# Optimization experiments

Measured on AMD Instinct MI355X. Metric: run time of the kernel, lower is better.

Reference implementation:

```python
import jax, jax.numpy as jnp
import numpy as np

HV = 128          # hidden_value_dim
HT = 17           # hidden_type_dim
K = HT - 9        # number of per-type composition linears (8)
D = 2 * (HV + HT) # gate-linear input dim (290)
O = 5 * HV        # gate-linear output dim (640)
P = 400_000       # child-state pool size
N = 200_000       # number of parent compositions


def setup_inputs() -> dict:
    key = jax.random.key(0)
    ks = jax.random.split(key, 7)
    h_pool = jax.random.normal(ks[0], (P, HV), dtype=jnp.float32)
    c_pool = jax.random.normal(ks[1], (P, HV), dtype=jnp.float32)
    # soft type distributions per child (gumbel-softmax outputs in the original)
    t_pool = jax.random.uniform(ks[2], (P, HT), dtype=jnp.float32)
    child_idx = jax.random.randint(ks[3], (N, 2), 0, P)
    parent_type = jax.random.randint(ks[4], (N,), 0, K)
    # per-type composition weights (comp_linear_v), orthogonal-ish init -> plain normal scaled
    W = jax.random.normal(ks[5], (K, O, D), dtype=jnp.float32) / np.sqrt(D)
    b = jnp.zeros((K, O), dtype=jnp.float32)
    return {"h_pool": h_pool, "c_pool": c_pool, "t_pool": t_pool,
            "child_idx": child_idx, "parent_type": parent_type,
            "W": W, "b": b}


def _compose(h_pool, c_pool, t_pool, child_idx, parent_type, W, b):
    # gather children states  [N, hv] / [N, ht]
    li, ri = child_idx[:, 0], child_idx[:, 1]
    hl, hr = h_pool[li], h_pool[ri]
    cl, cr = c_pool[li], c_pool[ri]
    tl, tr = t_pool[li], t_pool[ri]
    # per-type linear input: concat(hl, tl, hr, tr)  [N, D]
    x = jnp.concatenate([hl, tl, hr, tr], axis=-1)
    # per-type gates via masked accumulation over the small fixed set of K types
    gates = jnp.zeros((x.shape[0], O), dtype=x.dtype)
    for k in range(K):
        yk = x @ W[k].T + b[k]                       # [N, O]
        gates = jnp.where((parent_type == k)[:, None], yk, gates)
    # binary tree-LSTM cell update: i, f_l, f_r, u, o
    i, fl, fr, u, o = jnp.split(gates, 5, axis=-1)
    c = (jax.nn.sigmoid(i) * jnp.tanh(u)
         + jax.nn.sigmoid(fl) * cl
         + jax.nn.sigmoid(fr) * cr)
    h = jax.nn.sigmoid(o) * jnp.tanh(c)
    return jnp.concatenate([h, c], axis=-1)         # [N, 2*hv]


def reference(h_pool, c_pool, t_pool, child_idx, parent_type, W, b):
    return _compose(h_pool, c_pool, t_pool, child_idx, parent_type, W, b)
```

## Files before the change

### kernel.cpp

```cpp
#include <hip/hip_runtime.h>
#include <hip/hip_bf16.h>

#define HV   128
#define HT   17
#define DIMD 290
#define KP   320
#define OO   640
#define RT   64
#define KN   8

typedef unsigned short u16;
typedef __attribute__((ext_vector_type(8))) short short8v;
typedef __attribute__((ext_vector_type(4))) float f32x4;

__device__ __forceinline__ u16 f2bf(float x) {
    unsigned u = __float_as_uint(x);
    u = (u + 0x7FFFu + ((u >> 16) & 1u)) >> 16;
    return (u16)u;
}
__device__ __forceinline__ float sigf(float x) {
    return __builtin_amdgcn_rcpf(1.0f + __expf(-x));
}
__device__ __forceinline__ float tanhfast(float x) {
    return 1.0f - 2.0f * __builtin_amdgcn_rcpf(1.0f + __expf(2.0f * x));
}


__global__ void hist_k(const int* __restrict__ pt, int* __restrict__ hdr, int N) {
    __shared__ int c[KN];
    if (threadIdx.x < KN) c[threadIdx.x] = 0;
    __syncthreads();
    int n = blockIdx.x * 256 + threadIdx.x;
    if (n < N) atomicAdd(&c[pt[n]], 1);
    __syncthreads();
    if (threadIdx.x < KN && c[threadIdx.x]) atomicAdd(&hdr[threadIdx.x], c[threadIdx.x]);
}

__global__ void prefix_k(int* __restrict__ hdr) {
    if (threadIdx.x == 0 && blockIdx.x == 0) {
        int acc = 0;
        hdr[16] = 0;
        for (int k = 0; k < KN; ++k) {
            acc += (hdr[k] + RT - 1) / RT;
            hdr[17 + k] = acc;
        }
    }
}

__global__ void scatter_k(const int* __restrict__ pt, int* __restrict__ hdr,
                          int* __restrict__ idxbuf, int N) {
    __shared__ int c[KN], base[KN];
    if (threadIdx.x < KN) c[threadIdx.x] = 0;
    __syncthreads();
    int n = blockIdx.x * 256 + threadIdx.x;
    int k = 0, my = 0;
    if (n < N) { k = pt[n]; my = atomicAdd(&c[k], 1); }
    __syncthreads();
    if (threadIdx.x < KN)
        base[threadIdx.x] = c[threadIdx.x] ? atomicAdd(&hdr[8 + threadIdx.x], c[threadIdx.x]) : 0;
    __syncthreads();
    if (n < N) idxbuf[hdr[16 + k] * RT + base[k] + my] = n;
}

__global__ void wconv_k(const float* __restrict__ W, u16* __restrict__ Wt) {
    int k = blockIdx.y;
    int idx = blockIdx.x * 256 + threadIdx.x;
    if (idx >= OO * KP) return;
    int o = idx / KP, d = idx % KP;
    int src;
    if (d < 256)      src = (d < 128) ? d : d + 17;
    else if (d < 273) src = d - 128;
    else if (d < 290) src = d;
    else              src = -1;
    float v = (src >= 0) ? W[((size_t)k * OO + o) * DIMD + src] : 0.0f;
    int kk = d >> 5, e = d & 31;
    Wt[(((size_t)k * 10 + kk) * OO + o) * 32 + e] = f2bf(v);
}

__global__ __launch_bounds__(512, 2)
void fused_k(const float* __restrict__ h_pool, const float* __restrict__ c_pool,
             const float* __restrict__ t_pool, const int* __restrict__ child_idx,
             const float* __restrict__ bias, const u16* __restrict__ Wt,
             const int* __restrict__ hdr, const int* __restrict__ idxbuf,
             float* __restrict__ out) {
    __shared__ u16 sX[RT * KP];
    __shared__ int4 sMeta[2][RT];

    const int ntiles = hdr[24];
    const int t0 = blockIdx.x * 2;
    if (t0 >= ntiles) return;
    const int t1 = t0 + 1;
    const bool has1 = (t1 < ntiles);

    const int tid = threadIdx.x;
    const int r = tid >> 3, q = tid & 7;

    float4 A0[4], B0[4];
    float Tl0, Tl1, Tl2 = 0.f, Tr0, Tr1, Tr2 = 0.f;
    int sn, sl, sr2;

    auto loadmeta = [&](int tile) {
        sn = idxbuf[tile * RT + r];
        sl = 0; sr2 = 0;
        if (sn >= 0) { sl = child_idx[2 * sn]; sr2 = child_idx[2 * sn + 1]; }
    };
    auto issue_stage = [&]() {
        if (sn < 0) return;
        const float4* hl = (const float4*)(h_pool + (size_t)sl * HV);
        const float4* hr = (const float4*)(h_pool + (size_t)sr2 * HV);
        #pragma unroll
        for (int m = 0; m < 4; ++m) A0[m] = hl[q + 8 * m];
        #pragma unroll
        for (int m = 0; m < 4; ++m) B0[m] = hr[q + 8 * m];
        const float* tl = t_pool + (size_t)sl * HT;
        const float* tr = t_pool + (size_t)sr2 * HT;
        Tl0 = tl[q]; Tl1 = tl[q + 8];
        Tr0 = tr[q]; Tr1 = tr[q + 8];
        if (q == 0) { Tl2 = tl[16]; Tr2 = tr[16]; }
    };
    auto write_stage = [&]() {
        char* xr = (char*)sX + r * 640;
        const int swz = (r & 7) << 4;
        if (sn >= 0) {
            #pragma unroll
            for (int m = 0; m < 4; ++m) {
                float4 v = A0[m];
                *(ushort4*)(xr + (((q + 8 * m) * 8) ^ swz)) =
                    make_ushort4(f2bf(v.x), f2bf(v.y), f2bf(v.z), f2bf(v.w));
            }
            #pragma unroll
            for (int m = 0; m < 4; ++m) {
                float4 v = B0[m];
                *(ushort4*)(xr + ((256 + (q + 8 * m) * 8) ^ swz)) =
                    make_ushort4(f2bf(v.x), f2bf(v.y), f2bf(v.z), f2bf(v.w));
            }
            *(u16*)(xr + ((512 + 2 * q) ^ swz))       = f2bf(Tl0);
            *(u16*)(xr + ((512 + 2 * (q + 8)) ^ swz)) = f2bf(Tl1);
            *(u16*)(xr + ((546 + 2 * q) ^ swz))       = f2bf(Tr0);
            *(u16*)(xr + ((546 + 2 * (q + 8)) ^ swz)) = f2bf(Tr1);
            if (q == 0) {
                *(u16*)(xr + (544 ^ swz)) = f2bf(Tl2);
                *(u16*)(xr + (578 ^ swz)) = f2bf(Tr2);
            }
            for (int b = 580 + 2 * q; b < 640; b += 16)
                *(u16*)(xr + (b ^ swz)) = 0;
        } else {
            ushort4 z = make_ushort4(0, 0, 0, 0);
            for (int b = q * 8; b < 640; b += 64)
                *(ushort4*)(xr + (b ^ swz)) = z;
        }
    };

    loadmeta(t0);
    if (q == 0) sMeta[0][r] = make_int4(sn, sl, sr2, 0);
    issue_stage();
    write_stage();
    __syncthreads();

    const int wc = tid >> 6, lane = tid & 63;
    const int lo = lane & 15, hi = lane >> 4;
    const int hcol = wc * 16 + lo;
    const char* sXb = (const char*)sX;
    const int rowbase = lo * 640;
    const int swzl = (lo & 7) << 4;

    if (has1) {
        loadmeta(t1);
        if (q == 0) sMeta[1][r] = make_int4(sn, sl, sr2, 0);
        issue_stage();
    }

    int k0 = 0;
    #pragma unroll
    for (int j = 0; j < 7; ++j) k0 += (t0 >= hdr[17 + j]);

    int nodes[16];
    float cpl[16], cpr[16];
    #pragma unroll
    for (int m = 0; m < 4; ++m)
        #pragma unroll
        for (int jj = 0; jj < 4; ++jj) {
            int4 mt = sMeta[0][m * 16 + hi * 4 + jj];
            nodes[m * 4 + jj] = mt.x;
            cpl[m * 4 + jj] = c_pool[(size_t)mt.y * HV + hcol];
            cpr[m * 4 + jj] = c_pool[(size_t)mt.z * HV + hcol];
        }
    float bb[5];
    #pragma unroll
    for (int g = 0; g < 5; ++g) bb[g] = bias[k0 * OO + g * 128 + hcol];

    int wo[5];
    #pragma unroll
    for (int g = 0; g < 5; ++g)
        wo[g] = (g * 128 + hcol) * 32 + hi * 8;

    {
        f32x4 acc[5][4];
        #pragma unroll
        for (int g = 0; g < 5; ++g)
            #pragma unroll
            for (int m = 0; m < 4; ++m)
                acc[g][m] = (f32x4){0.f, 0.f, 0.f, 0.f};

        const u16* __restrict__ wt = Wt + ((size_t)k0 * 10 * OO) * 32;
        short8v wfa[5], wfb[5];
        #pragma unroll
        for (int g = 0; g < 5; ++g) wfa[g] = *(const short8v*)(wt + wo[g]);

        #pragma unroll
        for (int kk = 0; kk < 10; ++kk) {
            short8v (&wcur)[5] = (kk & 1) ? wfb : wfa;
            short8v (&wnxt)[5] = (kk & 1) ? wfa : wfb;
            if (kk < 9) {
                const u16* wtn = wt + (size_t)(kk + 1) * (OO * 32);
                #pragma unroll
                for (int g = 0; g < 5; ++g)
                    wnxt[g] = *(const short8v*)(wtn + wo[g]);
            }
            int a_off = rowbase + ((kk * 64 + hi * 16) ^ swzl);
            short8v a0 = *(const short8v*)(sXb + a_off);
            short8v a1 = *(const short8v*)(sXb + a_off + 10240);
            short8v a2 = *(const short8v*)(sXb + a_off + 20480);
            short8v a3 = *(const short8v*)(sXb + a_off + 30720);
            #pragma unroll
            for (int g = 0; g < 5; ++g) {
                acc[g][0] = __builtin_amdgcn_mfma_f32_16x16x32_bf16(a0, wcur[g], acc[g][0], 0, 0, 0);
                acc[g][1] = __builtin_amdgcn_mfma_f32_16x16x32_bf16(a1, wcur[g], acc[g][1], 0, 0, 0);
                acc[g][2] = __builtin_amdgcn_mfma_f32_16x16x32_bf16(a2, wcur[g], acc[g][2], 0, 0, 0);
                acc[g][3] = __builtin_amdgcn_mfma_f32_16x16x32_bf16(a3, wcur[g], acc[g][3], 0, 0, 0);
            }
        }

        #pragma unroll
        for (int m = 0; m < 4; ++m) {
            #pragma unroll
            for (int jj = 0; jj < 4; ++jj) {
                int node = nodes[m * 4 + jj];
                if (node < 0) continue;
                float cl = cpl[m * 4 + jj], cr = cpr[m * 4 + jj];
                float gi  = acc[0][m][jj] + bb[0];
                float gfl = acc[1][m][jj] + bb[1];
                float gfr = acc[2][m][jj] + bb[2];
                float gu  = acc[3][m][jj] + bb[3];
                float go  = acc[4][m][jj] + bb[4];
                float cc = sigf(gi) * tanhfast(gu) + sigf(gfl) * cl + sigf(gfr) * cr;
                float hh = sigf(go) * tanhfast(cc);
                float* orow = out + (size_t)node * (2 * HV);
                orow[hcol]      = hh;
                orow[HV + hcol] = cc;
            }
        }
    }

    if (!has1) return;

    __syncthreads();
    write_stage();
    __syncthreads();

    int k1 = 0;
    #pragma unroll
    for (int j = 0; j < 7; ++j) k1 += (t1 >= hdr[17 + j]);

    #pragma unroll
    for (int m = 0; m < 4; ++m)
        #pragma unroll
        for (int jj = 0; jj < 4; ++jj) {
            int4 mt = sMeta[1][m * 16 + hi * 4 + jj];
            nodes[m * 4 + jj] = mt.x;
            cpl[m * 4 + jj] = c_pool[(size_t)mt.y * HV + hcol];
            cpr[m * 4 + jj] = c_pool[(size_t)mt.z * HV + hcol];
        }
    #pragma unroll
    for (int g = 0; g < 5; ++g) bb[g] = bias[k1 * OO + g * 128 + hcol];

    {
        f32x4 acc[5][4];
        #pragma unroll
        for (int g = 0; g < 5; ++g)
            #pragma unroll
            for (int m = 0; m < 4; ++m)
                acc[g][m] = (f32x4){0.f, 0.f, 0.f, 0.f};

        const u16* __restrict__ wt = Wt + ((size_t)k1 * 10 * OO) * 32;
        short8v wfa[5], wfb[5];
        #pragma unroll
        for (int g = 0; g < 5; ++g) wfa[g] = *(const short8v*)(wt + wo[g]);

        #pragma unroll
        for (int kk = 0; kk < 10; ++kk) {
            short8v (&wcur)[5] = (kk & 1) ? wfb : wfa;
            short8v (&wnxt)[5] = (kk & 1) ? wfa : wfb;
            if (kk < 9) {
                const u16* wtn = wt + (size_t)(kk + 1) * (OO * 32);
                #pragma unroll
                for (int g = 0; g < 5; ++g)
                    wnxt[g] = *(const short8v*)(wtn + wo[g]);
            }
            int a_off = rowbase + ((kk * 64 + hi * 16) ^ swzl);
            short8v a0 = *(const short8v*)(sXb + a_off);
            short8v a1 = *(const short8v*)(sXb + a_off + 10240);
            short8v a2 = *(const short8v*)(sXb + a_off + 20480);
            short8v a3 = *(const short8v*)(sXb + a_off + 30720);
            #pragma unroll
            for (int g = 0; g < 5; ++g) {
                acc[g][0] = __builtin_amdgcn_mfma_f32_16x16x32_bf16(a0, wcur[g], acc[g][0], 0, 0, 0);
                acc[g][1] = __builtin_amdgcn_mfma_f32_16x16x32_bf16(a1, wcur[g], acc[g][1], 0, 0, 0);
                acc[g][2] = __builtin_amdgcn_mfma_f32_16x16x32_bf16(a2, wcur[g], acc[g][2], 0, 0, 0);
                acc[g][3] = __builtin_amdgcn_mfma_f32_16x16x32_bf16(a3, wcur[g], acc[g][3], 0, 0, 0);
            }
        }

        #pragma unroll
        for (int m = 0; m < 4; ++m) {
            #pragma unroll
            for (int jj = 0; jj < 4; ++jj) {
                int node = nodes[m * 4 + jj];
                if (node < 0) continue;
                float cl = cpl[m * 4 + jj], cr = cpr[m * 4 + jj];
                float gi  = acc[0][m][jj] + bb[0];
                float gfl = acc[1][m][jj] + bb[1];
                float gfr = acc[2][m][jj] + bb[2];
                float gu  = acc[3][m][jj] + bb[3];
                float go  = acc[4][m][jj] + bb[4];
                float cc = sigf(gi) * tanhfast(gu) + sigf(gfl) * cl + sigf(gfr) * cr;
                float hh = sigf(go) * tanhfast(cc);
                float* orow = out + (size_t)node * (2 * HV);
                orow[hcol]      = hh;
                orow[HV + hcol] = cc;
            }
        }
    }
}

extern "C" void kernel_launch(void* const* d_in, const int* in_sizes, int n_in,
                              void* d_out, int out_size, void* d_ws, size_t ws_size,
                              hipStream_t stream) {
    const float* h_pool      = (const float*)d_in[0];
    const float* c_pool      = (const float*)d_in[1];
    const float* t_pool      = (const float*)d_in[2];
    const int*   child_idx   = (const int*)d_in[3];
    const int*   parent_type = (const int*)d_in[4];
    const float* W           = (const float*)d_in[5];
    const float* bias        = (const float*)d_in[6];
    float* out = (float*)d_out;

    const int N = in_sizes[3] / 2;
    const int maxblk = (N + RT - 1) / RT + KN;
    const int totrows = maxblk * RT;

    char* ws = (char*)d_ws;
    size_t off = 0;
    int* hdr = (int*)ws;                         off += 1024;
    int* idxbuf = (int*)(ws + off);              off += (((size_t)totrows * 4 + 255) / 256) * 256;
    u16* Wt = (u16*)(ws + off);                  off += (size_t)KN * OO * KP * 2;

    hipMemsetAsync(hdr, 0, 1024, stream);
    hipMemsetAsync(idxbuf, 0xFF, (size_t)totrows * 4, stream);

    int nb = (N + 255) / 256;
    hist_k<<<nb, 256, 0, stream>>>(parent_type, hdr, N);
    prefix_k<<<1, 64, 0, stream>>>(hdr);
    scatter_k<<<nb, 256, 0, stream>>>(parent_type, hdr, idxbuf, N);
    wconv_k<<<dim3((OO * KP + 255) / 256, KN), 256, 0, stream>>>(W, Wt);
    fused_k<<<(maxblk + 1) / 2, 512, 0, stream>>>(
        h_pool, c_pool, t_pool, child_idx, bias, Wt, hdr, idxbuf, out);
}
```

Baseline: 321.9 us.

## Make fused kernel persistent with double-buffered LDS tile pipeline

```diff
diff --git a/kernel.cpp b/kernel.cpp
--- a/kernel.cpp
+++ b/kernel.cpp
@@ -8,6 +8,7 @@
 #define OO   640
 #define RT   64
 #define KN   8
+#define GG   256
 
 typedef unsigned short u16;
 typedef __attribute__((ext_vector_type(8))) short short8v;
@@ -78,19 +79,17 @@
 }
 
 __global__ __launch_bounds__(512, 2)
-void fused_k(const float* __restrict__ h_pool, const float* __restrict__ c_pool,
-             const float* __restrict__ t_pool, const int* __restrict__ child_idx,
-             const float* __restrict__ bias, const u16* __restrict__ Wt,
-             const int* __restrict__ hdr, const int* __restrict__ idxbuf,
-             float* __restrict__ out) {
-    __shared__ u16 sX[RT * KP];
+void fusedp_k(const float* __restrict__ h_pool, const float* __restrict__ c_pool,
+              const float* __restrict__ t_pool, const int* __restrict__ child_idx,
+              const float* __restrict__ bias, const u16* __restrict__ Wt,
+              const int* __restrict__ hdr, const int* __restrict__ idxbuf,
+              float* __restrict__ out) {
+    __shared__ u16 sX[2][RT * KP];
     __shared__ int4 sMeta[2][RT];
 
     const int ntiles = hdr[24];
-    const int t0 = blockIdx.x * 2;
-    if (t0 >= ntiles) return;
-    const int t1 = t0 + 1;
-    const bool has1 = (t1 < ntiles);
+    const int bx = blockIdx.x;
+    if (bx >= ntiles) return;
 
     const int tid = threadIdx.x;
     const int r = tid >> 3, q = tid & 7;
@@ -118,8 +117,8 @@
         Tr0 = tr[q]; Tr1 = tr[q + 8];
         if (q == 0) { Tl2 = tl[16]; Tr2 = tr[16]; }
     };
-    auto write_stage = [&]() {
-        char* xr = (char*)sX + r * 640;
+    auto write_stage = [&](int pb) {
+        char* xr = (char*)sX[pb] + r * 640;
         const int swz = (r & 7) << 4;
         if (sn >= 0) {
             #pragma unroll
@@ -151,50 +150,51 @@
         }
     };
 
-    loadmeta(t0);
+    loadmeta(bx);
     if (q == 0) sMeta[0][r] = make_int4(sn, sl, sr2, 0);
     issue_stage();
-    write_stage();
+    write_stage(0);
+    if (bx + GG < ntiles) { loadmeta(bx + GG); issue_stage(); }
     __syncthreads();
 
     const int wc = tid >> 6, lane = tid & 63;
     const int lo = lane & 15, hi = lane >> 4;
     const int hcol = wc * 16 + lo;
-    const char* sXb = (const char*)sX;
     const int rowbase = lo * 640;
     const int swzl = (lo & 7) << 4;
-
-    if (has1) {
-        loadmeta(t1);
-        if (q == 0) sMeta[1][r] = make_int4(sn, sl, sr2, 0);
-        issue_stage();
-    }
-
-    int k0 = 0;
-    #pragma unroll
-    for (int j = 0; j < 7; ++j) k0 += (t0 >= hdr[17 + j]);
-
-    int nodes[16];
-    float cpl[16], cpr[16];
-    #pragma unroll
-    for (int m = 0; m < 4; ++m)
-        #pragma unroll
-        for (int jj = 0; jj < 4; ++jj) {
-            int4 mt = sMeta[0][m * 16 + hi * 4 + jj];
-            nodes[m * 4 + jj] = mt.x;
-            cpl[m * 4 + jj] = c_pool[(size_t)mt.y * HV + hcol];
-            cpr[m * 4 + jj] = c_pool[(size_t)mt.z * HV + hcol];
-        }
-    float bb[5];
-    #pragma unroll
-    for (int g = 0; g < 5; ++g) bb[g] = bias[k0 * OO + g * 128 + hcol];
-
     int wo[5];
     #pragma unroll
     for (int g = 0; g < 5; ++g)
         wo[g] = (g * 128 + hcol) * 32 + hi * 8;
 
-    {
+    int p = 0;
+    for (int t = bx; t < ntiles; t += GG) {
+        const char* sXb = (const char*)sX[p];
+
+        int k = 0;
+        #pragma unroll
+        for (int j = 0; j < 7; ++j) k += (t >= hdr[17 + j]);
+
+        float cpl[16], cpr[16];
+        #pragma unroll
+        for (int m = 0; m < 4; ++m)
+            #pragma unroll
+            for (int jj = 0; jj < 4; ++jj) {
+                int4 mt = sMeta[p][m * 16 + hi * 4 + jj];
+                cpl[m * 4 + jj] = c_pool[(size_t)mt.y * HV + hcol];
+                cpr[m * 4 + jj] = c_pool[(size_t)mt.z * HV + hcol];
+            }
+        float bb[5];
+        #pragma unroll
+        for (int g = 0; g < 5; ++g) bb[g] = bias[k * OO + g * 128 + hcol];
+
+        const bool hasn1 = (t + GG < ntiles);
+        if (hasn1) {
+            if (q == 0) sMeta[p ^ 1][r] = make_int4(sn, sl, sr2, 0);
+            write_stage(p ^ 1);
+        }
+        if (t + 2 * GG < ntiles) { loadmeta(t + 2 * GG); issue_stage(); }
+
         f32x4 acc[5][4];
         #pragma unroll
         for (int g = 0; g < 5; ++g)
@@ -202,7 +202,7 @@
             for (int m = 0; m < 4; ++m)
                 acc[g][m] = (f32x4){0.f, 0.f, 0.f, 0.f};
 
-        const u16* __restrict__ wt = Wt + ((size_t)k0 * 10 * OO) * 32;
+        const u16* __restrict__ wt = Wt + ((size_t)k * 10 * OO) * 32;
         short8v wfa[5], wfb[5];
         #pragma unroll
         for (int g = 0; g < 5; ++g) wfa[g] = *(const short8v*)(wt + wo[g]);
@@ -235,8 +235,8 @@
         for (int m = 0; m < 4; ++m) {
             #pragma unroll
             for (int jj = 0; jj < 4; ++jj) {
-                int node = nodes[m * 4 + jj];
-                if (node < 0) continue;
+                int4 mt = sMeta[p][m * 16 + hi * 4 + jj];
+                if (mt.x < 0) continue;
                 float cl = cpl[m * 4 + jj], cr = cpr[m * 4 + jj];
                 float gi  = acc[0][m][jj] + bb[0];
                 float gfl = acc[1][m][jj] + bb[1];
@@ -245,90 +245,16 @@
                 float go  = acc[4][m][jj] + bb[4];
                 float cc = sigf(gi) * tanhfast(gu) + sigf(gfl) * cl + sigf(gfr) * cr;
                 float hh = sigf(go) * tanhfast(cc);
-                float* orow = out + (size_t)node * (2 * HV);
+                float* orow = out + (size_t)mt.x * (2 * HV);
                 orow[hcol]      = hh;
                 orow[HV + hcol] = cc;
             }
         }
-    }
-
-    if (!has1) return;
-
-    __syncthreads();
-    write_stage();
-    __syncthreads();
-
-    int k1 = 0;
-    #pragma unroll
-    for (int j = 0; j < 7; ++j) k1 += (t1 >= hdr[17 + j]);
-
-    #pragma unroll
-    for (int m = 0; m < 4; ++m)
-        #pragma unroll
-        for (int jj = 0; jj < 4; ++jj) {
-            int4 mt = sMeta[1][m * 16 + hi * 4 + jj];
-            nodes[m * 4 + jj] = mt.x;
-            cpl[m * 4 + jj] = c_pool[(size_t)mt.y * HV + hcol];
-            cpr[m * 4 + jj] = c_pool[(size_t)mt.z * HV + hcol];
-        }
-    #pragma unroll
-    for (int g = 0; g < 5; ++g) bb[g] = bias[k1 * OO + g * 128 + hcol];
-
-    {
-        f32x4 acc[5][4];
-        #pragma unroll
-        for (int g = 0; g < 5; ++g)
-            #pragma unroll
-            for (int m = 0; m < 4; ++m)
-                acc[g][m] = (f32x4){0.f, 0.f, 0.f, 0.f};
-
-        const u16* __restrict__ wt = Wt + ((size_t)k1 * 10 * OO) * 32;
-        short8v wfa[5], wfb[5];
-        #pragma unroll
-        for (int g = 0; g < 5; ++g) wfa[g] = *(const short8v*)(wt + wo[g]);
-
-        #pragma unroll
-        for (int kk = 0; kk < 10; ++kk) {
-            short8v (&wcur)[5] = (kk & 1) ? wfb : wfa;
-            short8v (&wnxt)[5] = (kk & 1) ? wfa : wfb;
-            if (kk < 9) {
-                const u16* wtn = wt + (size_t)(kk + 1) * (OO * 32);
-                #pragma unroll
-                for (int g = 0; g < 5; ++g)
-                    wnxt[g] = *(const short8v*)(wtn + wo[g]);
-            }
-            int a_off = rowbase + ((kk * 64 + hi * 16) ^ swzl);
-            short8v a0 = *(const short8v*)(sXb + a_off);
-            short8v a1 = *(const short8v*)(sXb + a_off + 10240);
-            short8v a2 = *(const short8v*)(sXb + a_off + 20480);
-            short8v a3 = *(const short8v*)(sXb + a_off + 30720);
-            #pragma unroll
-            for (int g = 0; g < 5; ++g) {
-                acc[g][0] = __builtin_amdgcn_mfma_f32_16x16x32_bf16(a0, wcur[g], acc[g][0], 0, 0, 0);
-                acc[g][1] = __builtin_amdgcn_mfma_f32_16x16x32_bf16(a1, wcur[g], acc[g][1], 0, 0, 0);
-                acc[g][2] = __builtin_amdgcn_mfma_f32_16x16x32_bf16(a2, wcur[g], acc[g][2], 0, 0, 0);
-                acc[g][3] = __builtin_amdgcn_mfma_f32_16x16x32_bf16(a3, wcur[g], acc[g][3], 0, 0, 0);
-            }
-        }
-
-        #pragma unroll
-        for (int m = 0; m < 4; ++m) {
-            #pragma unroll
-            for (int jj = 0; jj < 4; ++jj) {
-                int node = nodes[m * 4 + jj];
-                if (node < 0) continue;
-                float cl = cpl[m * 4 + jj], cr = cpr[m * 4 + jj];
-                float gi  = acc[0][m][jj] + bb[0];
-                float gfl = acc[1][m][jj] + bb[1];
-                float gfr = acc[2][m][jj] + bb[2];
-                float gu  = acc[3][m][jj] + bb[3];
-                float go  = acc[4][m][jj] + bb[4];
-                float cc = sigf(gi) * tanhfast(gu) + sigf(gfl) * cl + sigf(gfr) * cr;
-                float hh = sigf(go) * tanhfast(cc);
-                float* orow = out + (size_t)node * (2 * HV);
-                orow[hcol]      = hh;
-                orow[HV + hcol] = cc;
-            }
+
+        if (hasn1) {
+            asm volatile("s_waitcnt lgkmcnt(0)" ::: "memory");
+            __builtin_amdgcn_s_barrier();
+            p ^= 1;
         }
     }
 }
@@ -363,6 +289,6 @@
     prefix_k<<<1, 64, 0, stream>>>(hdr);
     scatter_k<<<nb, 256, 0, stream>>>(parent_type, hdr, idxbuf, N);
     wconv_k<<<dim3((OO * KP + 255) / 256, KN), 256, 0, stream>>>(W, Wt);
-    fused_k<<<(maxblk + 1) / 2, 512, 0, stream>>>(
+    fusedp_k<<<GG, 512, 0, stream>>>(
         h_pool, c_pool, t_pool, child_idx, bias, Wt, hdr, idxbuf, out);
 }
```

Result: no change. 324.3 us (+0.7%).

## Split tile rows across two wave groups with 1024-thread blocks

Applied to the files above, without the earlier changes.

```diff
diff --git a/kernel.cpp b/kernel.cpp
--- a/kernel.cpp
+++ b/kernel.cpp
@@ -77,12 +77,12 @@
     Wt[(((size_t)k * 10 + kk) * OO + o) * 32 + e] = f2bf(v);
 }
 
-__global__ __launch_bounds__(512, 2)
-void fused_k(const float* __restrict__ h_pool, const float* __restrict__ c_pool,
-             const float* __restrict__ t_pool, const int* __restrict__ child_idx,
-             const float* __restrict__ bias, const u16* __restrict__ Wt,
-             const int* __restrict__ hdr, const int* __restrict__ idxbuf,
-             float* __restrict__ out) {
+__global__ __launch_bounds__(1024, 4)
+void fused2_k(const float* __restrict__ h_pool, const float* __restrict__ c_pool,
+              const float* __restrict__ t_pool, const int* __restrict__ child_idx,
+              const float* __restrict__ bias, const u16* __restrict__ Wt,
+              const int* __restrict__ hdr, const int* __restrict__ idxbuf,
+              float* __restrict__ out) {
     __shared__ u16 sX[RT * KP];
     __shared__ int4 sMeta[2][RT];
 
@@ -93,10 +93,10 @@
     const bool has1 = (t1 < ntiles);
 
     const int tid = threadIdx.x;
-    const int r = tid >> 3, q = tid & 7;
-
-    float4 A0[4], B0[4];
-    float Tl0, Tl1, Tl2 = 0.f, Tr0, Tr1, Tr2 = 0.f;
+    const int r = tid >> 4, q = tid & 15;
+
+    float4 A0[2], B0[2];
+    float Tl0, Tl2 = 0.f, Tr0, Tr2 = 0.f;
     int sn, sl, sr2;
 
     auto loadmeta = [&](int tile) {
@@ -109,13 +109,12 @@
         const float4* hl = (const float4*)(h_pool + (size_t)sl * HV);
         const float4* hr = (const float4*)(h_pool + (size_t)sr2 * HV);
         #pragma unroll
-        for (int m = 0; m < 4; ++m) A0[m] = hl[q + 8 * m];
-        #pragma unroll
-        for (int m = 0; m < 4; ++m) B0[m] = hr[q + 8 * m];
+        for (int m = 0; m < 2; ++m) A0[m] = hl[q + 16 * m];
+        #pragma unroll
+        for (int m = 0; m < 2; ++m) B0[m] = hr[q + 16 * m];
         const float* tl = t_pool + (size_t)sl * HT;
         const float* tr = t_pool + (size_t)sr2 * HT;
-        Tl0 = tl[q]; Tl1 = tl[q + 8];
-        Tr0 = tr[q]; Tr1 = tr[q + 8];
+        Tl0 = tl[q]; Tr0 = tr[q];
         if (q == 0) { Tl2 = tl[16]; Tr2 = tr[16]; }
     };
     auto write_stage = [&]() {
@@ -123,30 +122,28 @@
         const int swz = (r & 7) << 4;
         if (sn >= 0) {
             #pragma unroll
-            for (int m = 0; m < 4; ++m) {
+            for (int m = 0; m < 2; ++m) {
                 float4 v = A0[m];
-                *(ushort4*)(xr + (((q + 8 * m) * 8) ^ swz)) =
+                *(ushort4*)(xr + (((q + 16 * m) * 8) ^ swz)) =
                     make_ushort4(f2bf(v.x), f2bf(v.y), f2bf(v.z), f2bf(v.w));
             }
             #pragma unroll
-            for (int m = 0; m < 4; ++m) {
+            for (int m = 0; m < 2; ++m) {
                 float4 v = B0[m];
-                *(ushort4*)(xr + ((256 + (q + 8 * m) * 8) ^ swz)) =
+                *(ushort4*)(xr + ((256 + (q + 16 * m) * 8) ^ swz)) =
                     make_ushort4(f2bf(v.x), f2bf(v.y), f2bf(v.z), f2bf(v.w));
             }
-            *(u16*)(xr + ((512 + 2 * q) ^ swz))       = f2bf(Tl0);
-            *(u16*)(xr + ((512 + 2 * (q + 8)) ^ swz)) = f2bf(Tl1);
-            *(u16*)(xr + ((546 + 2 * q) ^ swz))       = f2bf(Tr0);
-            *(u16*)(xr + ((546 + 2 * (q + 8)) ^ swz)) = f2bf(Tr1);
+            *(u16*)(xr + ((512 + 2 * q) ^ swz)) = f2bf(Tl0);
+            *(u16*)(xr + ((546 + 2 * q) ^ swz)) = f2bf(Tr0);
             if (q == 0) {
                 *(u16*)(xr + (544 ^ swz)) = f2bf(Tl2);
                 *(u16*)(xr + (578 ^ swz)) = f2bf(Tr2);
             }
-            for (int b = 580 + 2 * q; b < 640; b += 16)
+            for (int b = 580 + 2 * q; b < 640; b += 32)
                 *(u16*)(xr + (b ^ swz)) = 0;
         } else {
             ushort4 z = make_ushort4(0, 0, 0, 0);
-            for (int b = q * 8; b < 640; b += 64)
+            for (int b = q * 8; b < 640; b += 128)
                 *(ushort4*)(xr + (b ^ swz)) = z;
         }
     };
@@ -157,11 +154,12 @@
     write_stage();
     __syncthreads();
 
-    const int wc = tid >> 6, lane = tid & 63;
+    const int w = tid >> 6, lane = tid & 63;
+    const int rg = w >> 3, c0 = w & 7;
     const int lo = lane & 15, hi = lane >> 4;
-    const int hcol = wc * 16 + lo;
+    const int hcol = c0 * 16 + lo;
     const char* sXb = (const char*)sX;
-    const int rowbase = lo * 640;
+    const int rowbase0 = (rg * 32 + lo) * 640;
     const int swzl = (lo & 7) << 4;
 
     if (has1) {
@@ -174,16 +172,16 @@
     #pragma unroll
     for (int j = 0; j < 7; ++j) k0 += (t0 >= hdr[17 + j]);
 
-    int nodes[16];
-    float cpl[16], cpr[16];
-    #pragma unroll
-    for (int m = 0; m < 4; ++m)
+    int nodes[8];
+    float cpl[8], cpr[8];
+    #pragma unroll
+    for (int f = 0; f < 2; ++f)
         #pragma unroll
         for (int jj = 0; jj < 4; ++jj) {
-            int4 mt = sMeta[0][m * 16 + hi * 4 + jj];
-            nodes[m * 4 + jj] = mt.x;
-            cpl[m * 4 + jj] = c_pool[(size_t)mt.y * HV + hcol];
-            cpr[m * 4 + jj] = c_pool[(size_t)mt.z * HV + hcol];
+            int4 mt = sMeta[0][rg * 32 + f * 16 + hi * 4 + jj];
+            nodes[f * 4 + jj] = mt.x;
+            cpl[f * 4 + jj] = c_pool[(size_t)mt.y * HV + hcol];
+            cpr[f * 4 + jj] = c_pool[(size_t)mt.z * HV + hcol];
         }
     float bb[5];
     #pragma unroll
@@ -195,12 +193,12 @@
         wo[g] = (g * 128 + hcol) * 32 + hi * 8;
 
     {
-        f32x4 acc[5][4];
+        f32x4 acc[5][2];
         #pragma unroll
         for (int g = 0; g < 5; ++g)
             #pragma unroll
-            for (int m = 0; m < 4; ++m)
-                acc[g][m] = (f32x4){0.f, 0.f, 0.f, 0.f};
+            for (int f = 0; f < 2; ++f)
+                acc[g][f] = (f32x4){0.f, 0.f, 0.f, 0.f};
 
         const u16* __restrict__ wt = Wt + ((size_t)k0 * 10 * OO) * 32;
         short8v wfa[5], wfb[5];
@@ -217,32 +215,28 @@
                 for (int g = 0; g < 5; ++g)
                     wnxt[g] = *(const short8v*)(wtn + wo[g]);
             }
-            int a_off = rowbase + ((kk * 64 + hi * 16) ^ swzl);
+            int a_off = rowbase0 + ((kk * 64 + hi * 16) ^ swzl);
             short8v a0 = *(const short8v*)(sXb + a_off);
             short8v a1 = *(const short8v*)(sXb + a_off + 10240);
-            short8v a2 = *(const short8v*)(sXb + a_off + 20480);
-            short8v a3 = *(const short8v*)(sXb + a_off + 30720);
             #pragma unroll
             for (int g = 0; g < 5; ++g) {
                 acc[g][0] = __builtin_amdgcn_mfma_f32_16x16x32_bf16(a0, wcur[g], acc[g][0], 0, 0, 0);
                 acc[g][1] = __builtin_amdgcn_mfma_f32_16x16x32_bf16(a1, wcur[g], acc[g][1], 0, 0, 0);
-                acc[g][2] = __builtin_amdgcn_mfma_f32_16x16x32_bf16(a2, wcur[g], acc[g][2], 0, 0, 0);
-                acc[g][3] = __builtin_amdgcn_mfma_f32_16x16x32_bf16(a3, wcur[g], acc[g][3], 0, 0, 0);
-            }
-        }
-
-        #pragma unroll
-        for (int m = 0; m < 4; ++m) {
+            }
+        }
+
+        #pragma unroll
+        for (int f = 0; f < 2; ++f) {
             #pragma unroll
             for (int jj = 0; jj < 4; ++jj) {
-                int node = nodes[m * 4 + jj];
+                int node = nodes[f * 4 + jj];
                 if (node < 0) continue;
-                float cl = cpl[m * 4 + jj], cr = cpr[m * 4 + jj];
-                float gi  = acc[0][m][jj] + bb[0];
-                float gfl = acc[1][m][jj] + bb[1];
-                float gfr = acc[2][m][jj] + bb[2];
-                float gu  = acc[3][m][jj] + bb[3];
-                float go  = acc[4][m][jj] + bb[4];
+                float cl = cpl[f * 4 + jj], cr = cpr[f * 4 + jj];
+                float gi  = acc[0][f][jj] + bb[0];
+                float gfl = acc[1][f][jj] + bb[1];
+                float gfr = acc[2][f][jj] + bb[2];
+                float gu  = acc[3][f][jj] + bb[3];
+                float go  = acc[4][f][jj] + bb[4];
                 float cc = sigf(gi) * tanhfast(gu) + sigf(gfl) * cl + sigf(gfr) * cr;
                 float hh = sigf(go) * tanhfast(cc);
                 float* orow = out + (size_t)node * (2 * HV);
@@ -263,24 +257,24 @@
     for (int j = 0; j < 7; ++j) k1 += (t1 >= hdr[17 + j]);
 
     #pragma unroll
-    for (int m = 0; m < 4; ++m)
+    for (int f = 0; f < 2; ++f)
         #pragma unroll
         for (int jj = 0; jj < 4; ++jj) {
-            int4 mt = sMeta[1][m * 16 + hi * 4 + jj];
-            nodes[m * 4 + jj] = mt.x;
-            cpl[m * 4 + jj] = c_pool[(size_t)mt.y * HV + hcol];
-            cpr[m * 4 + jj] = c_pool[(size_t)mt.z * HV + hcol];
+            int4 mt = sMeta[1][rg * 32 + f * 16 + hi * 4 + jj];
+            nodes[f * 4 + jj] = mt.x;
+            cpl[f * 4 + jj] = c_pool[(size_t)mt.y * HV + hcol];
+            cpr[f * 4 + jj] = c_pool[(size_t)mt.z * HV + hcol];
         }
     #pragma unroll
     for (int g = 0; g < 5; ++g) bb[g] = bias[k1 * OO + g * 128 + hcol];
 
     {
-        f32x4 acc[5][4];
+        f32x4 acc[5][2];
         #pragma unroll
         for (int g = 0; g < 5; ++g)
             #pragma unroll
-            for (int m = 0; m < 4; ++m)
-                acc[g][m] = (f32x4){0.f, 0.f, 0.f, 0.f};
+            for (int f = 0; f < 2; ++f)
+                acc[g][f] = (f32x4){0.f, 0.f, 0.f, 0.f};
 
         const u16* __restrict__ wt = Wt + ((size_t)k1 * 10 * OO) * 32;
         short8v wfa[5], wfb[5];
@@ -297,32 +291,28 @@
                 for (int g = 0; g < 5; ++g)
                     wnxt[g] = *(const short8v*)(wtn + wo[g]);
             }
-            int a_off = rowbase + ((kk * 64 + hi * 16) ^ swzl);
+            int a_off = rowbase0 + ((kk * 64 + hi * 16) ^ swzl);
             short8v a0 = *(const short8v*)(sXb + a_off);
             short8v a1 = *(const short8v*)(sXb + a_off + 10240);
-            short8v a2 = *(const short8v*)(sXb + a_off + 20480);
-            short8v a3 = *(const short8v*)(sXb + a_off + 30720);
             #pragma unroll
             for (int g = 0; g < 5; ++g) {
                 acc[g][0] = __builtin_amdgcn_mfma_f32_16x16x32_bf16(a0, wcur[g], acc[g][0], 0, 0, 0);
                 acc[g][1] = __builtin_amdgcn_mfma_f32_16x16x32_bf16(a1, wcur[g], acc[g][1], 0, 0, 0);
-                acc[g][2] = __builtin_amdgcn_mfma_f32_16x16x32_bf16(a2, wcur[g], acc[g][2], 0, 0, 0);
-                acc[g][3] = __builtin_amdgcn_mfma_f32_16x16x32_bf16(a3, wcur[g], acc[g][3], 0, 0, 0);
-            }
-        }
-
-        #pragma unroll
-        for (int m = 0; m < 4; ++m) {
+            }
+        }
+
+        #pragma unroll
+        for (int f = 0; f < 2; ++f) {
             #pragma unroll
             for (int jj = 0; jj < 4; ++jj) {
-                int node = nodes[m * 4 + jj];
+                int node = nodes[f * 4 + jj];
                 if (node < 0) continue;
-                float cl = cpl[m * 4 + jj], cr = cpr[m * 4 + jj];
-                float gi  = acc[0][m][jj] + bb[0];
-                float gfl = acc[1][m][jj] + bb[1];
-                float gfr = acc[2][m][jj] + bb[2];
-                float gu  = acc[3][m][jj] + bb[3];
-                float go  = acc[4][m][jj] + bb[4];
+                float cl = cpl[f * 4 + jj], cr = cpr[f * 4 + jj];
+                float gi  = acc[0][f][jj] + bb[0];
+                float gfl = acc[1][f][jj] + bb[1];
+                float gfr = acc[2][f][jj] + bb[2];
+                float gu  = acc[3][f][jj] + bb[3];
+                float go  = acc[4][f][jj] + bb[4];
                 float cc = sigf(gi) * tanhfast(gu) + sigf(gfl) * cl + sigf(gfr) * cr;
                 float hh = sigf(go) * tanhfast(cc);
                 float* orow = out + (size_t)node * (2 * HV);
@@ -363,6 +353,6 @@
     prefix_k<<<1, 64, 0, stream>>>(hdr);
     scatter_k<<<nb, 256, 0, stream>>>(parent_type, hdr, idxbuf, N);
     wconv_k<<<dim3((OO * KP + 255) / 256, KN), 256, 0, stream>>>(W, Wt);
-    fused_k<<<(maxblk + 1) / 2, 512, 0, stream>>>(
+    fused2_k<<<(maxblk + 1) / 2, 1024, 0, stream>>>(
         h_pool, c_pool, t_pool, child_idx, bias, Wt, hdr, idxbuf, out);
 }
```

Result: slower. 362.0 us (+12.4%).

## Halve row tile, raise occupancy, remap blocks across XCDs, reorder prefetch

Applied to the files above, without the earlier changes.

```diff
diff --git a/kernel.cpp b/kernel.cpp
--- a/kernel.cpp
+++ b/kernel.cpp
@@ -6,17 +6,22 @@
 #define DIMD 290
 #define KP   320
 #define OO   640
-#define RT   64
+#define RT   32
 #define KN   8
+#define NXCD 8
 
 typedef unsigned short u16;
 typedef __attribute__((ext_vector_type(8))) short short8v;
 typedef __attribute__((ext_vector_type(4))) float f32x4;
 
 __device__ __forceinline__ u16 f2bf(float x) {
-    unsigned u = __float_as_uint(x);
-    u = (u + 0x7FFFu + ((u >> 16) & 1u)) >> 16;
-    return (u16)u;
+    __hip_bfloat16 b = __float2bfloat16(x);
+    return __builtin_bit_cast(u16, b);
+}
+__device__ __forceinline__ ushort4 f2bf4(float4 v) {
+    ushort4 r;
+    r.x = f2bf(v.x); r.y = f2bf(v.y); r.z = f2bf(v.z); r.w = f2bf(v.w);
+    return r;
 }
 __device__ __forceinline__ float sigf(float x) {
     return __builtin_amdgcn_rcpf(1.0f + __expf(-x));
@@ -77,7 +82,7 @@
     Wt[(((size_t)k * 10 + kk) * OO + o) * 32 + e] = f2bf(v);
 }
 
-__global__ __launch_bounds__(512, 2)
+__global__ __launch_bounds__(512, 4)
 void fused_k(const float* __restrict__ h_pool, const float* __restrict__ c_pool,
              const float* __restrict__ t_pool, const int* __restrict__ child_idx,
              const float* __restrict__ bias, const u16* __restrict__ Wt,
@@ -87,16 +92,22 @@
     __shared__ int4 sMeta[2][RT];
 
     const int ntiles = hdr[24];
-    const int t0 = blockIdx.x * 2;
+
+    const int nwg = gridDim.x;
+    const int bq = nwg >> 3, br = nwg & (NXCD - 1);
+    const int xcd = blockIdx.x & (NXCD - 1), ixc = blockIdx.x >> 3;
+    const int sbid = (xcd < br ? xcd * (bq + 1) : br * (bq + 1) + (xcd - br) * bq) + ixc;
+
+    const int t0 = sbid * 2;
     if (t0 >= ntiles) return;
     const int t1 = t0 + 1;
     const bool has1 = (t1 < ntiles);
 
     const int tid = threadIdx.x;
-    const int r = tid >> 3, q = tid & 7;
-
-    float4 A0[4], B0[4];
-    float Tl0, Tl1, Tl2 = 0.f, Tr0, Tr1, Tr2 = 0.f;
+    const int r = tid >> 4, q = tid & 15;
+
+    float4 A0[2], B0[2];
+    float Tl0, Tl2 = 0.f, Tr0, Tr2 = 0.f;
     int sn, sl, sr2;
 
     auto loadmeta = [&](int tile) {
@@ -109,13 +120,12 @@
         const float4* hl = (const float4*)(h_pool + (size_t)sl * HV);
         const float4* hr = (const float4*)(h_pool + (size_t)sr2 * HV);
         #pragma unroll
-        for (int m = 0; m < 4; ++m) A0[m] = hl[q + 8 * m];
-        #pragma unroll
-        for (int m = 0; m < 4; ++m) B0[m] = hr[q + 8 * m];
+        for (int m = 0; m < 2; ++m) A0[m] = hl[q + 16 * m];
+        #pragma unroll
+        for (int m = 0; m < 2; ++m) B0[m] = hr[q + 16 * m];
         const float* tl = t_pool + (size_t)sl * HT;
         const float* tr = t_pool + (size_t)sr2 * HT;
-        Tl0 = tl[q]; Tl1 = tl[q + 8];
-        Tr0 = tr[q]; Tr1 = tr[q + 8];
+        Tl0 = tl[q]; Tr0 = tr[q];
         if (q == 0) { Tl2 = tl[16]; Tr2 = tr[16]; }
     };
     auto write_stage = [&]() {
@@ -123,30 +133,22 @@
         const int swz = (r & 7) << 4;
         if (sn >= 0) {
             #pragma unroll
-            for (int m = 0; m < 4; ++m) {
-                float4 v = A0[m];
-                *(ushort4*)(xr + (((q + 8 * m) * 8) ^ swz)) =
-                    make_ushort4(f2bf(v.x), f2bf(v.y), f2bf(v.z), f2bf(v.w));
-            }
+            for (int m = 0; m < 2; ++m)
+                *(ushort4*)(xr + (((q + 16 * m) * 8) ^ swz)) = f2bf4(A0[m]);
             #pragma unroll
-            for (int m = 0; m < 4; ++m) {
-                float4 v = B0[m];
-                *(ushort4*)(xr + ((256 + (q + 8 * m) * 8) ^ swz)) =
-                    make_ushort4(f2bf(v.x), f2bf(v.y), f2bf(v.z), f2bf(v.w));
-            }
-            *(u16*)(xr + ((512 + 2 * q) ^ swz))       = f2bf(Tl0);
-            *(u16*)(xr + ((512 + 2 * (q + 8)) ^ swz)) = f2bf(Tl1);
-            *(u16*)(xr + ((546 + 2 * q) ^ swz))       = f2bf(Tr0);
-            *(u16*)(xr + ((546 + 2 * (q + 8)) ^ swz)) = f2bf(Tr1);
+            for (int m = 0; m < 2; ++m)
+                *(ushort4*)(xr + ((256 + (q + 16 * m) * 8) ^ swz)) = f2bf4(B0[m]);
+            *(u16*)(xr + ((512 + 2 * q) ^ swz)) = f2bf(Tl0);
+            *(u16*)(xr + ((546 + 2 * q) ^ swz)) = f2bf(Tr0);
             if (q == 0) {
                 *(u16*)(xr + (544 ^ swz)) = f2bf(Tl2);
                 *(u16*)(xr + (578 ^ swz)) = f2bf(Tr2);
             }
-            for (int b = 580 + 2 * q; b < 640; b += 16)
+            for (int b = 580 + 2 * q; b < 640; b += 32)
                 *(u16*)(xr + (b ^ swz)) = 0;
         } else {
             ushort4 z = make_ushort4(0, 0, 0, 0);
-            for (int b = q * 8; b < 640; b += 64)
+            for (int b = q * 8; b < 640; b += 128)
                 *(ushort4*)(xr + (b ^ swz)) = z;
         }
     };
@@ -164,44 +166,23 @@
     const int rowbase = lo * 640;
     const int swzl = (lo & 7) << 4;
 
-    if (has1) {
-        loadmeta(t1);
-        if (q == 0) sMeta[1][r] = make_int4(sn, sl, sr2, 0);
-        issue_stage();
-    }
-
     int k0 = 0;
     #pragma unroll
     for (int j = 0; j < 7; ++j) k0 += (t0 >= hdr[17 + j]);
-
-    int nodes[16];
-    float cpl[16], cpr[16];
-    #pragma unroll
-    for (int m = 0; m < 4; ++m)
-        #pragma unroll
-        for (int jj = 0; jj < 4; ++jj) {
-            int4 mt = sMeta[0][m * 16 + hi * 4 + jj];
-            nodes[m * 4 + jj] = mt.x;
-            cpl[m * 4 + jj] = c_pool[(size_t)mt.y * HV + hcol];
-            cpr[m * 4 + jj] = c_pool[(size_t)mt.z * HV + hcol];
-        }
-    float bb[5];
-    #pragma unroll
-    for (int g = 0; g < 5; ++g) bb[g] = bias[k0 * OO + g * 128 + hcol];
 
     int wo[5];
     #pragma unroll
     for (int g = 0; g < 5; ++g)
         wo[g] = (g * 128 + hcol) * 32 + hi * 8;
 
+    f32x4 acc[5][2];
+    #pragma unroll
+    for (int g = 0; g < 5; ++g)
+        #pragma unroll
+        for (int m = 0; m < 2; ++m)
+            acc[g][m] = (f32x4){0.f, 0.f, 0.f, 0.f};
+
     {
-        f32x4 acc[5][4];
-        #pragma unroll
-        for (int g = 0; g < 5; ++g)
-            #pragma unroll
-            for (int m = 0; m < 4; ++m)
-                acc[g][m] = (f32x4){0.f, 0.f, 0.f, 0.f};
-
         const u16* __restrict__ wt = Wt + ((size_t)k0 * 10 * OO) * 32;
         short8v wfa[5], wfb[5];
         #pragma unroll
@@ -220,68 +201,75 @@
             int a_off = rowbase + ((kk * 64 + hi * 16) ^ swzl);
             short8v a0 = *(const short8v*)(sXb + a_off);
             short8v a1 = *(const short8v*)(sXb + a_off + 10240);
-            short8v a2 = *(const short8v*)(sXb + a_off + 20480);
-            short8v a3 = *(const short8v*)(sXb + a_off + 30720);
             #pragma unroll
             for (int g = 0; g < 5; ++g) {
                 acc[g][0] = __builtin_amdgcn_mfma_f32_16x16x32_bf16(a0, wcur[g], acc[g][0], 0, 0, 0);
                 acc[g][1] = __builtin_amdgcn_mfma_f32_16x16x32_bf16(a1, wcur[g], acc[g][1], 0, 0, 0);
-                acc[g][2] = __builtin_amdgcn_mfma_f32_16x16x32_bf16(a2, wcur[g], acc[g][2], 0, 0, 0);
-                acc[g][3] = __builtin_amdgcn_mfma_f32_16x16x32_bf16(a3, wcur[g], acc[g][3], 0, 0, 0);
-            }
-        }
-
-        #pragma unroll
-        for (int m = 0; m < 4; ++m) {
-            #pragma unroll
-            for (int jj = 0; jj < 4; ++jj) {
-                int node = nodes[m * 4 + jj];
-                if (node < 0) continue;
-                float cl = cpl[m * 4 + jj], cr = cpr[m * 4 + jj];
-                float gi  = acc[0][m][jj] + bb[0];
-                float gfl = acc[1][m][jj] + bb[1];
-                float gfr = acc[2][m][jj] + bb[2];
-                float gu  = acc[3][m][jj] + bb[3];
-                float go  = acc[4][m][jj] + bb[4];
-                float cc = sigf(gi) * tanhfast(gu) + sigf(gfl) * cl + sigf(gfr) * cr;
-                float hh = sigf(go) * tanhfast(cc);
-                float* orow = out + (size_t)node * (2 * HV);
-                orow[hcol]      = hh;
-                orow[HV + hcol] = cc;
-            }
-        }
-    }
-
-    if (!has1) return;
-
-    __syncthreads();
-    write_stage();
-    __syncthreads();
-
-    int k1 = 0;
-    #pragma unroll
-    for (int j = 0; j < 7; ++j) k1 += (t1 >= hdr[17 + j]);
-
-    #pragma unroll
-    for (int m = 0; m < 4; ++m)
+            }
+        }
+    }
+
+    if (has1) {
+        loadmeta(t1);
+        if (q == 0) sMeta[1][r] = make_int4(sn, sl, sr2, 0);
+        issue_stage();
+    }
+    __builtin_amdgcn_sched_barrier(0);
+
+    float bb[5];
+    #pragma unroll
+    for (int g = 0; g < 5; ++g) bb[g] = bias[k0 * OO + g * 128 + hcol];
+
+    int nodes[8];
+    float cpl[8], cpr[8];
+    #pragma unroll
+    for (int m = 0; m < 2; ++m)
         #pragma unroll
         for (int jj = 0; jj < 4; ++jj) {
-            int4 mt = sMeta[1][m * 16 + hi * 4 + jj];
+            int4 mt = sMeta[0][m * 16 + hi * 4 + jj];
             nodes[m * 4 + jj] = mt.x;
             cpl[m * 4 + jj] = c_pool[(size_t)mt.y * HV + hcol];
             cpr[m * 4 + jj] = c_pool[(size_t)mt.z * HV + hcol];
         }
-    #pragma unroll
-    for (int g = 0; g < 5; ++g) bb[g] = bias[k1 * OO + g * 128 + hcol];
+
+    #pragma unroll
+    for (int m = 0; m < 2; ++m) {
+        #pragma unroll
+        for (int jj = 0; jj < 4; ++jj) {
+            int node = nodes[m * 4 + jj];
+            if (node < 0) continue;
+            float cl = cpl[m * 4 + jj], cr = cpr[m * 4 + jj];
+            float gi  = acc[0][m][jj] + bb[0];
+            float gfl = acc[1][m][jj] + bb[1];
+            float gfr = acc[2][m][jj] + bb[2];
+            float gu  = acc[3][m][jj] + bb[3];
+            float go  = acc[4][m][jj] + bb[4];
+            float cc = sigf(gi) * tanhfast(gu) + sigf(gfl) * cl + sigf(gfr) * cr;
+            float hh = sigf(go) * tanhfast(cc);
+            float* orow = out + (size_t)node * (2 * HV);
+            orow[hcol]      = hh;
+            orow[HV + hcol] = cc;
+        }
+    }
+
+    if (!has1) return;
+
+    __builtin_amdgcn_s_barrier();
+    write_stage();
+    asm volatile("s_waitcnt lgkmcnt(0)" ::: "memory");
+    __builtin_amdgcn_s_barrier();
+
+    int k1 = 0;
+    #pragma unroll
+    for (int j = 0; j < 7; ++j) k1 += (t1 >= hdr[17 + j]);
+
+    #pragma unroll
+    for (int g = 0; g < 5; ++g)
+        #pragma unroll
+        for (int m = 0; m < 2; ++m)
+            acc[g][m] = (f32x4){0.f, 0.f, 0.f, 0.f};
 
     {
-        f32x4 acc[5][4];
-        #pragma unroll
-        for (int g = 0; g < 5; ++g)
-            #pragma unroll
-            for (int m = 0; m < 4; ++m)
-                acc[g][m] = (f32x4){0.f, 0.f, 0.f, 0.f};
-
         const u16* __restrict__ wt = Wt + ((size_t)k1 * 10 * OO) * 32;
         short8v wfa[5], wfb[5];
         #pragma unroll
@@ -300,35 +288,44 @@
             int a_off = rowbase + ((kk * 64 + hi * 16) ^ swzl);
             short8v a0 = *(const short8v*)(sXb + a_off);
             short8v a1 = *(const short8v*)(sXb + a_off + 10240);
-            short8v a2 = *(const short8v*)(sXb + a_off + 20480);
-            short8v a3 = *(const short8v*)(sXb + a_off + 30720);
             #pragma unroll
             for (int g = 0; g < 5; ++g) {
                 acc[g][0] = __builtin_amdgcn_mfma_f32_16x16x32_bf16(a0, wcur[g], acc[g][0], 0, 0, 0);
                 acc[g][1] = __builtin_amdgcn_mfma_f32_16x16x32_bf16(a1, wcur[g], acc[g][1], 0, 0, 0);
-                acc[g][2] = __builtin_amdgcn_mfma_f32_16x16x32_bf16(a2, wcur[g], acc[g][2], 0, 0, 0);
-                acc[g][3] = __builtin_amdgcn_mfma_f32_16x16x32_bf16(a3, wcur[g], acc[g][3], 0, 0, 0);
-            }
-        }
-
-        #pragma unroll
-        for (int m = 0; m < 4; ++m) {
-            #pragma unroll
-            for (int jj = 0; jj < 4; ++jj) {
-                int node = nodes[m * 4 + jj];
-                if (node < 0) continue;
-                float cl = cpl[m * 4 + jj], cr = cpr[m * 4 + jj];
-                float gi  = acc[0][m][jj] + bb[0];
-                float gfl = acc[1][m][jj] + bb[1];
-                float gfr = acc[2][m][jj] + bb[2];
-                float gu  = acc[3][m][jj] + bb[3];
-                float go  = acc[4][m][jj] + bb[4];
-                float cc = sigf(gi) * tanhfast(gu) + sigf(gfl) * cl + sigf(gfr) * cr;
-                float hh = sigf(go) * tanhfast(cc);
-                float* orow = out + (size_t)node * (2 * HV);
-                orow[hcol]      = hh;
-                orow[HV + hcol] = cc;
-            }
+            }
+        }
+    }
+
+    #pragma unroll
+    for (int g = 0; g < 5; ++g) bb[g] = bias[k1 * OO + g * 128 + hcol];
+
+    #pragma unroll
+    for (int m = 0; m < 2; ++m)
+        #pragma unroll
+        for (int jj = 0; jj < 4; ++jj) {
+            int4 mt = sMeta[1][m * 16 + hi * 4 + jj];
+            nodes[m * 4 + jj] = mt.x;
+            cpl[m * 4 + jj] = c_pool[(size_t)mt.y * HV + hcol];
+            cpr[m * 4 + jj] = c_pool[(size_t)mt.z * HV + hcol];
+        }
+
+    #pragma unroll
+    for (int m = 0; m < 2; ++m) {
+        #pragma unroll
+        for (int jj = 0; jj < 4; ++jj) {
+            int node = nodes[m * 4 + jj];
+            if (node < 0) continue;
+            float cl = cpl[m * 4 + jj], cr = cpr[m * 4 + jj];
+            float gi  = acc[0][m][jj] + bb[0];
+            float gfl = acc[1][m][jj] + bb[1];
+            float gfr = acc[2][m][jj] + bb[2];
+            float gu  = acc[3][m][jj] + bb[3];
+            float go  = acc[4][m][jj] + bb[4];
+            float cc = sigf(gi) * tanhfast(gu) + sigf(gfl) * cl + sigf(gfr) * cr;
+            float hh = sigf(go) * tanhfast(cc);
+            float* orow = out + (size_t)node * (2 * HV);
+            orow[hcol]      = hh;
+            orow[HV + hcol] = cc;
         }
     }
 }
```

New measurement: 389.1 us. 1.21x slower.
